# Performance work log

Measured on AMD Instinct MI355X. Metric: run time of the kernel, lower is better.

Reference implementation:

```python
import jax, jax.numpy as jnp
import numpy as np

B, S, D, H = 2, 2048, 1024, 16
DH = D // H
EPS = 1e-5


def setup_inputs() -> dict:
    key = jax.random.key(0)
    ks = jax.random.split(key, 12)
    inp = {
        "Q_source": jax.random.normal(ks[0], (B, S, D), jnp.float32),
        "K_source": jax.random.normal(ks[1], (B, S, D), jnp.float32),
        "V_source": jax.random.normal(ks[2], (B, S, D), jnp.float32),
        "padding_mask": jnp.zeros((B, 1, 1, S), dtype=bool),  # no padded keys (avoids NaN rows)
        "future_mask": jnp.triu(jnp.ones((S, S), dtype=bool), k=1)[None, None],  # causal
    }
    sc = 1.0 / np.sqrt(D)
    names = ["WQ", "WK", "WV", "WO"]
    for i, n in enumerate(names):
        inp[n] = jax.random.normal(ks[3 + i], (D, D), jnp.float32) * sc
        inp["b" + n[1]] = jnp.zeros((D,), jnp.float32)
    inp["gamma"] = jnp.ones((D,), jnp.float32)
    inp["beta"] = jnp.zeros((D,), jnp.float32)
    return inp


def reference(Q_source, K_source, V_source, padding_mask, future_mask,
              WQ, bQ, WK, bK, WV, bV, WO, bO, gamma, beta):
    b = Q_source.shape[0]
    # torch Linear: x @ W.T + b ; reshape to [B, H, S, DH]
    def proj(x, W, bb):
        y = x @ W.T + bb
        return y.reshape(b, -1, H, DH).transpose(0, 2, 1, 3)

    Q = proj(Q_source, WQ, bQ)
    K = proj(K_source, WK, bK)
    V = proj(V_source, WV, bV)

    scores = jnp.einsum("bhqd,bhkd->bhqk", Q, K) / jnp.sqrt(jnp.float32(DH))
    neg_inf = jnp.float32(-jnp.inf)
    scores = jnp.where(padding_mask, neg_inf, scores)
    scores = jnp.where(future_mask, neg_inf, scores)
    attn = jax.nn.softmax(scores, axis=-1)

    ctx = jnp.einsum("bhqk,bhkd->bhqd", attn, V)
    ctx = ctx.transpose(0, 2, 1, 3).reshape(b, -1, D)
    out = ctx @ WO.T + bO

    x = Q_source + out
    mu = x.mean(-1, keepdims=True)
    var = x.var(-1, keepdims=True)
    return (x - mu) * jax.lax.rsqrt(var + EPS) * gamma + beta
```

## Files before the change

### kernel.cpp

```cpp
#include <hip/hip_runtime.h>

#define S_LEN 2048
#define DMODEL 1024
#define NH 16
#define DHD 64

typedef __attribute__((ext_vector_type(8))) short bh8;
typedef __attribute__((ext_vector_type(4))) float f32x4;
typedef __attribute__((ext_vector_type(2))) unsigned int u32x2;
typedef __attribute__((ext_vector_type(4))) unsigned int u32x4;
typedef unsigned short u16;
typedef unsigned int u32;

static __device__ __forceinline__ u16 f2bf(float f) {
    unsigned u = __builtin_bit_cast(unsigned, f);
    u += 0x7fffu + ((u >> 16) & 1u);
    return (u16)(u >> 16);
}

typedef const __attribute__((address_space(1))) void* gptr_t;
typedef __attribute__((address_space(3))) void* lptr_t;

static __device__ __forceinline__ void gll16(const void* g, void* l) {
    __builtin_amdgcn_global_load_lds((gptr_t)g, (lptr_t)l, 16, 0, 0);
}

__global__ __launch_bounds__(256) void cvt_all(const float* __restrict__ WQ, const float* __restrict__ WK,
                                               const float* __restrict__ WV, const float* __restrict__ WO,
                                               const float* __restrict__ S0, const float* __restrict__ S1,
                                               const float* __restrict__ S2,
                                               u16* __restrict__ wq, u16* __restrict__ wk,
                                               u16* __restrict__ wv, u16* __restrict__ wo,
                                               u16* __restrict__ q0, u16* __restrict__ k0,
                                               u16* __restrict__ v0) {
    int bid = blockIdx.x;
    const float* s;
    u16* o;
    size_t base;
    if (bid < 2048) {
        int wi = bid >> 9;
        s = wi == 0 ? WQ : (wi == 1 ? WK : (wi == 2 ? WV : WO));
        o = wi == 0 ? wq : (wi == 1 ? wk : (wi == 2 ? wv : wo));
        base = (size_t)(bid & 511) * 2048;
    } else {
        int r = bid - 2048;
        int si = r >> 11;
        s = si == 0 ? S0 : (si == 1 ? S1 : S2);
        o = si == 0 ? q0 : (si == 1 ? k0 : v0);
        base = (size_t)(r & 2047) * 2048;
    }
    size_t i = base + (size_t)threadIdx.x * 8;
    float4 a = *(const float4*)(s + i);
    float4 b = *(const float4*)(s + i + 4);
    u32 p0 = (u32)f2bf(a.x) | ((u32)f2bf(a.y) << 16);
    u32 p1 = (u32)f2bf(a.z) | ((u32)f2bf(a.w) << 16);
    u32 p2 = (u32)f2bf(b.x) | ((u32)f2bf(b.y) << 16);
    u32 p3 = (u32)f2bf(b.z) | ((u32)f2bf(b.w) << 16);
    *(u32x4*)(o + i) = (u32x4){p0, p1, p2, p3};
}

template <int BM, int OBF, int AF32>
static __device__ __forceinline__ void gemm_body(const void* __restrict__ Ap, const u16* __restrict__ Bm,
                                                 const float* __restrict__ bias, void* __restrict__ Cv,
                                                 int N, int K, int bi, int bj, short* Al, short* Bl,
                                                 float oscale) {
    constexpr int MI = BM / 32;
    constexpr int NC = BM / 64;
    int tid = threadIdx.x, lane = tid & 63, w = tid >> 6;
    int ln = lane & 15, hi = lane >> 4;
    int wm = w >> 1, wn = w & 1;
    f32x4 acc[MI][4];
#pragma unroll
    for (int i = 0; i < MI; i++)
#pragma unroll
        for (int j = 0; j < 4; j++) acc[i][j] = (f32x4){0.f, 0.f, 0.f, 0.f};
    int nk = K >> 5;

    float4 fa[NC][2];
    auto loadA = [&](int kt) {
#pragma unroll
        for (int c = 0; c < NC; ++c) {
            int o = c * 4096 + tid * 16;
            int row = o >> 6, e0 = (o & 63) >> 1;
            const float* src = (const float*)Ap + (size_t)(bi * BM + row) * K + kt * 32 + e0;
            fa[c][0] = *(const float4*)src;
            fa[c][1] = *(const float4*)(src + 4);
        }
    };
    auto writeA = [&](int buf) {
#pragma unroll
        for (int c = 0; c < NC; ++c) {
            int o = c * 4096 + tid * 16;
            u32 w0 = (u32)f2bf(fa[c][0].x) | ((u32)f2bf(fa[c][0].y) << 16);
            u32 w1 = (u32)f2bf(fa[c][0].z) | ((u32)f2bf(fa[c][0].w) << 16);
            u32 w2 = (u32)f2bf(fa[c][1].x) | ((u32)f2bf(fa[c][1].y) << 16);
            u32 w3 = (u32)f2bf(fa[c][1].z) | ((u32)f2bf(fa[c][1].w) << 16);
            *(u32x4*)((char*)(Al + buf * (BM * 32)) + o) = (u32x4){w0, w1, w2, w3};
        }
    };
    auto stageA_lds = [&](int buf, int kt) {
#pragma unroll
        for (int c = 0; c < NC; ++c) {
            int o = c * 4096 + tid * 16;
            int row = o >> 6, col = (o & 63) >> 1;
            gll16((const u16*)Ap + (size_t)(bi * BM + row) * K + kt * 32 + col,
                  (char*)(Al + buf * (BM * 32)) + o);
        }
    };
    auto stageB = [&](int buf, int kt) {
#pragma unroll
        for (int c = 0; c < 2; ++c) {
            int o = c * 4096 + tid * 16;
            int row = o >> 6, col = (o & 63) >> 1;
            gll16(Bm + (size_t)(bj * 128 + row) * K + kt * 32 + col, (char*)(Bl + buf * 4096) + o);
        }
    };

    if constexpr (AF32) { loadA(0); writeA(0); } else { stageA_lds(0, 0); }
    stageB(0, 0);
    __syncthreads();
    int cur = 0;
    for (int kt = 0; kt < nk; ++kt) {
        bool pre = (kt + 1 < nk);
        if (pre) {
            if constexpr (AF32) loadA(kt + 1); else stageA_lds(cur ^ 1, kt + 1);
            stageB(cur ^ 1, kt + 1);
        }
        bh8 av[MI], bv[4];
#pragma unroll
        for (int i = 0; i < MI; i++) av[i] = *(const bh8*)&Al[cur * (BM * 32) + (wm * (BM / 2) + i * 16 + ln) * 32 + hi * 8];
#pragma unroll
        for (int j = 0; j < 4; j++) bv[j] = *(const bh8*)&Bl[cur * 4096 + (wn * 64 + j * 16 + ln) * 32 + hi * 8];
#pragma unroll
        for (int i = 0; i < MI; i++)
#pragma unroll
            for (int j = 0; j < 4; j++)
                acc[i][j] = __builtin_amdgcn_mfma_f32_16x16x32_bf16(av[i], bv[j], acc[i][j], 0, 0, 0);
        if constexpr (AF32) { if (pre) writeA(cur ^ 1); }
        __syncthreads();
        cur ^= 1;
    }
    if constexpr (OBF == 2) {
#pragma unroll
        for (int j = 0; j < 4; j++) {
            int col = wn * 64 + j * 16 + ln;
            float bvs = bias[bj * 128 + col];
#pragma unroll
            for (int i = 0; i < MI; i++) {
                int row0 = wm * (BM / 2) + i * 16 + hi * 4;
                u32 p01 = (u32)f2bf(acc[i][j][0] + bvs) | ((u32)f2bf(acc[i][j][1] + bvs) << 16);
                u32 p23 = (u32)f2bf(acc[i][j][2] + bvs) | ((u32)f2bf(acc[i][j][3] + bvs) << 16);
                int idx = col * 128 + (row0 ^ ((col & 7) << 3));
                *(u32x2*)&Al[idx] = (u32x2){p01, p23};
            }
        }
        __syncthreads();
        int b = bi >> 4;
        int sbase = (bi & 15) * 128;
#pragma unroll
        for (int it = 0; it < 8; ++it) {
            int idx = it * 256 + tid;
            int dcol = idx >> 4;
            int sl = (idx & 15) * 8;
            bh8 v = *(const bh8*)&Al[dcol * 128 + (sl ^ ((dcol & 7) << 3))];
            int h = bj * 2 + (dcol >> 6), d = dcol & 63;
            *(bh8*)((u16*)Cv + ((size_t)((b * 16 + h) * 64 + d)) * 2048 + sbase + sl) = v;
        }
        return;
    }
#pragma unroll
    for (int j = 0; j < 4; j++) {
        int col = bj * 128 + wn * 64 + j * 16 + ln;
        float bvs = bias[col];
#pragma unroll
        for (int i = 0; i < MI; i++) {
            int row0 = bi * BM + wm * (BM / 2) + i * 16 + hi * 4;
#pragma unroll
            for (int rr = 0; rr < 4; rr++) {
                if (OBF) {
                    float v = (acc[i][j][rr] + bvs) * oscale;
                    ((u16*)Cv)[(size_t)(row0 + rr) * N + col] = f2bf(v);
                } else {
                    ((float*)Cv)[(size_t)(row0 + rr) * N + col] = acc[i][j][rr] + bvs;
                }
            }
        }
    }
}

__global__ __launch_bounds__(256, 3) void gemm_qkv(const u16* __restrict__ A0, const u16* __restrict__ A1,
                                                   const u16* __restrict__ A2, const u16* __restrict__ B0,
                                                   const u16* __restrict__ B1, const u16* __restrict__ B2,
                                                   const float* __restrict__ c0, const float* __restrict__ c1,
                                                   const float* __restrict__ c2, u16* __restrict__ C0,
                                                   u16* __restrict__ C1, u16* __restrict__ VT) {
    __shared__ short SH[16384];
    short* Al = SH;
    short* Bl = SH + 8192;
    int bid = blockIdx.x;
    int swz = (bid & 7) * 96 + (bid >> 3);
    int z = swz >> 8, t = swz & 255;
    if (z == 2) {
        gemm_body<128, 2, 0>(A2, B2, c2, VT, 1024, 1024, t >> 3, t & 7, Al, Bl, 1.0f);
    } else if (z == 0) {
        gemm_body<128, 1, 0>(A0, B0, c0, C0, 1024, 1024, t >> 3, t & 7, Al, Bl, 0.18033688f);
    } else {
        gemm_body<128, 1, 0>(A1, B1, c1, C1, 1024, 1024, t >> 3, t & 7, Al, Bl, 1.0f);
    }
}

__global__ __launch_bounds__(256) void gemm_o(const u16* __restrict__ A, const u16* __restrict__ Bm,
                                              const float* __restrict__ bias, float* __restrict__ C) {
    __shared__ short Al[2 * 64 * 32];
    __shared__ short Bl[2 * 128 * 32];
    int bid = blockIdx.x;
    int swz = (bid & 7) * 64 + (bid >> 3);
    gemm_body<64, 0, 0>(A, Bm, bias, C, 1024, 1024, swz >> 3, swz & 7, Al, Bl, 1.0f);
}

template <int PLO, int PHI>
static __device__ __forceinline__ void attn_core(const u16* __restrict__ Qp, const u16* __restrict__ Kp,
                                                 const u16* __restrict__ VT, u16* __restrict__ Ctx,
                                                 short* Klb, short* Vlb, short* Pw,
                                                 int b, int h, int bh, int qt, int tid) {
    int lane = tid & 63, w = tid >> 6;
    int ln = lane & 15, hi = lane >> 4;
    __builtin_amdgcn_s_setprio(PLO);
    bh8 ones;
#pragma unroll
    for (int e = 0; e < 8; e++) ones[e] = (short)0x3F80;

    auto stage_kv = [&](int buf, int kt) {
#pragma unroll
        for (int c = 0; c < 2; ++c) {
            int o = c * 4096 + tid * 16;
            int r = o >> 7;
            int slot = (o >> 4) & 7;
            gll16(Kp + ((size_t)(b * S_LEN + kt * 64 + r)) * DMODEL + h * DHD + ((slot ^ (r & 7)) << 3),
                  (char*)(Klb + buf * 4096) + o);
            gll16(VT + ((size_t)(bh * DHD + r)) * S_LEN + kt * 64 + ((slot ^ (r & 7)) << 3),
                  (char*)(Vlb + buf * 4096) + o);
        }
    };

    int nt = qt + 1;
    int qg = (qt << 6) + w * 16 + ln;
    const bh8* qrow = (const bh8*)(Qp + ((size_t)(b * S_LEN + qg)) * DMODEL + h * DHD);
    bh8 qf0 = qrow[hi], qf1 = qrow[4 + hi];
    f32x4 ctxa[4];
    f32x4 lacc = (f32x4){0.f, 0.f, 0.f, 0.f};
#pragma unroll
    for (int i = 0; i < 4; i++) ctxa[i] = (f32x4){0.f, 0.f, 0.f, 0.f};
    stage_kv(0, 0);
    __syncthreads();
    int cur = 0;
    for (int kt = 0; kt < nt; ++kt) {
        if (kt + 1 < nt) stage_kv(cur ^ 1, kt + 1);
        f32x4 sc[4];
#pragma unroll
        for (int ks = 0; ks < 4; ++ks) sc[ks] = (f32x4){0.f, 0.f, 0.f, 0.f};
        __builtin_amdgcn_s_setprio(PHI);
#pragma unroll
        for (int dwin = 0; dwin < 2; ++dwin) {
            bh8 qv = dwin ? qf1 : qf0;
#pragma unroll
            for (int ks = 0; ks < 4; ++ks) {
                int r = ks * 16 + ln;
                bh8 kv = *(const bh8*)&Klb[cur * 4096 + r * 64 + ((dwin * 32 + hi * 8) ^ ((r & 7) << 3))];
                sc[ks] = __builtin_amdgcn_mfma_f32_16x16x32_bf16(kv, qv, sc[ks], 0, 0, 0);
            }
        }
        __builtin_amdgcn_s_setprio(PLO);
        if (kt == nt - 1) {
#pragma unroll
            for (int ks = 0; ks < 4; ++ks)
#pragma unroll
                for (int rr = 0; rr < 4; ++rr) {
                    int kg = kt * 64 + ks * 16 + hi * 4 + rr;
                    sc[ks][rr] = (kg <= qg) ? sc[ks][rr] : -1e30f;
                }
        }
#pragma unroll
        for (int ks = 0; ks < 4; ++ks) {
            u32 u0 = __builtin_bit_cast(u32, __builtin_amdgcn_exp2f(sc[ks][0]));
            u32 u1 = __builtin_bit_cast(u32, __builtin_amdgcn_exp2f(sc[ks][1]));
            u32 u2 = __builtin_bit_cast(u32, __builtin_amdgcn_exp2f(sc[ks][2]));
            u32 u3 = __builtin_bit_cast(u32, __builtin_amdgcn_exp2f(sc[ks][3]));
            u32 a01 = (u0 >> 16) | (u1 & 0xffff0000u);
            u32 a23 = (u2 >> 16) | (u3 & 0xffff0000u);
            int kloc = ks * 16 + hi * 4;
            *(u32x2*)&Pw[ln * 64 + (kloc ^ ((ln & 7) << 3))] = (u32x2){a01, a23};
        }
        __builtin_amdgcn_s_setprio(PHI);
#pragma unroll
        for (int kw = 0; kw < 2; ++kw) {
            bh8 pf = *(const bh8*)&Pw[ln * 64 + ((kw * 32 + hi * 8) ^ ((ln & 7) << 3))];
            lacc = __builtin_amdgcn_mfma_f32_16x16x32_bf16(ones, pf, lacc, 0, 0, 0);
#pragma unroll
            for (int ds = 0; ds < 4; ++ds) {
                int d = ds * 16 + ln;
                bh8 vf = *(const bh8*)&Vlb[cur * 4096 + d * 64 + ((kw * 32 + hi * 8) ^ ((d & 7) << 3))];
                ctxa[ds] = __builtin_amdgcn_mfma_f32_16x16x32_bf16(vf, pf, ctxa[ds], 0, 0, 0);
            }
        }
        __builtin_amdgcn_s_setprio(PLO);
        __syncthreads();
        cur ^= 1;
    }
    float inv = 1.f / lacc[0];
    u16* cp = Ctx + ((size_t)(b * S_LEN + qg)) * DMODEL + h * DHD;
#pragma unroll
    for (int ds = 0; ds < 4; ++ds) {
        ushort4 st;
        st.x = f2bf(ctxa[ds][0] * inv);
        st.y = f2bf(ctxa[ds][1] * inv);
        st.z = f2bf(ctxa[ds][2] * inv);
        st.w = f2bf(ctxa[ds][3] * inv);
        *(ushort4*)(cp + ds * 16 + hi * 4) = st;
    }
    __builtin_amdgcn_s_setprio(0);
}

__global__ __launch_bounds__(256) void attn_fwd(const u16* __restrict__ Qp, const u16* __restrict__ Kp,
                                                const u16* __restrict__ VT, u16* __restrict__ Ctx) {
    __shared__ short Kl[2][64 * 64];
    __shared__ short Vl[2][64 * 64];
    __shared__ short Pl[4][16 * 64];
    int tid = threadIdx.x, w = tid >> 6;
    int bid = blockIdx.x;
    int xcd = bid & 7, j = bid >> 3;
    int rnd = j >> 5, cu = j & 31;
    int bh = xcd * 4 + (cu >> 4) + ((rnd >> 1) << 1);
    int qe = cu & 15;
    int qt = (rnd & 1) ? (31 - 2 * qe) : (2 * qe);
    int b = bh >> 4, h = bh & 15;
    if (qt >= 16)
        attn_core<2, 3>(Qp, Kp, VT, Ctx, &Kl[0][0], &Vl[0][0], &Pl[w][0], b, h, bh, qt, tid);
    else
        attn_core<0, 1>(Qp, Kp, VT, Ctx, &Kl[0][0], &Vl[0][0], &Pl[w][0], b, h, bh, qt, tid);
}

__global__ __launch_bounds__(256) void ln_res(const float* __restrict__ Xres, const float* __restrict__ Y,
                                              const float* __restrict__ gamma, const float* __restrict__ beta,
                                              float* __restrict__ out) {
    int row = blockIdx.x, tid = threadIdx.x;
    const float4* xr = (const float4*)(Xres + (size_t)row * DMODEL);
    const float4* yr = (const float4*)(Y + (size_t)row * DMODEL);
    float4 a = xr[tid], bq = yr[tid];
    float x0 = a.x + bq.x, x1 = a.y + bq.y, x2 = a.z + bq.z, x3 = a.w + bq.w;
    float s1 = x0 + x1 + x2 + x3;
    float s2 = x0 * x0 + x1 * x1 + x2 * x2 + x3 * x3;
#pragma unroll
    for (int off = 32; off > 0; off >>= 1) {
        s1 += __shfl_xor(s1, off);
        s2 += __shfl_xor(s2, off);
    }
    __shared__ float r1[4], r2[4];
    int wv = tid >> 6;
    if ((tid & 63) == 0) { r1[wv] = s1; r2[wv] = s2; }
    __syncthreads();
    s1 = r1[0] + r1[1] + r1[2] + r1[3];
    s2 = r2[0] + r2[1] + r2[2] + r2[3];
    float mu = s1 * (1.0f / 1024.0f);
    float var = s2 * (1.0f / 1024.0f) - mu * mu;
    float rstd = rsqrtf(var + 1e-5f);
    const float4* g4 = (const float4*)gamma;
    const float4* b4 = (const float4*)beta;
    float4 g = g4[tid], bb = b4[tid];
    float4 res;
    res.x = (x0 - mu) * rstd * g.x + bb.x;
    res.y = (x1 - mu) * rstd * g.y + bb.y;
    res.z = (x2 - mu) * rstd * g.z + bb.z;
    res.w = (x3 - mu) * rstd * g.w + bb.w;
    *((float4*)(out + (size_t)row * DMODEL) + tid) = res;
}

extern "C" void kernel_launch(void* const* d_in, const int* in_sizes, int n_in,
                              void* d_out, int out_size, void* d_ws, size_t ws_size,
                              hipStream_t stream) {
    const float* Qs = (const float*)d_in[0];
    const float* Ks = (const float*)d_in[1];
    const float* Vs = (const float*)d_in[2];
    const float* WQ = (const float*)d_in[5];
    const float* bQ = (const float*)d_in[6];
    const float* WK = (const float*)d_in[7];
    const float* bK = (const float*)d_in[8];
    const float* WV = (const float*)d_in[9];
    const float* bV = (const float*)d_in[10];
    const float* WO = (const float*)d_in[11];
    const float* bO = (const float*)d_in[12];
    const float* gamma = (const float*)d_in[13];
    const float* beta = (const float*)d_in[14];

    const size_t MB = 1u << 20;
    char* w8 = (char*)d_ws;
    u16* Qb  = (u16*)(w8 + 0 * MB);
    u16* Kb  = (u16*)(w8 + 8 * MB);
    u16* Vb  = (u16*)(w8 + 16 * MB);
    u16* WQb = (u16*)(w8 + 24 * MB);
    u16* WKb = (u16*)(w8 + 26 * MB);
    u16* WVb = (u16*)(w8 + 28 * MB);
    u16* WOb = (u16*)(w8 + 30 * MB);
    u16* Qp  = (u16*)(w8 + 32 * MB);
    u16* Kp  = (u16*)(w8 + 40 * MB);
    u16* VTb = (u16*)(w8 + 56 * MB);
    u16* Ctx = (u16*)(w8 + 64 * MB);
    float* Y2 = (float*)(w8 + 72 * MB);

    cvt_all<<<8192, 256, 0, stream>>>(WQ, WK, WV, WO, Qs, Ks, Vs, WQb, WKb, WVb, WOb, Qb, Kb, Vb);
    gemm_qkv<<<768, 256, 0, stream>>>(Qb, Kb, Vb, WQb, WKb, WVb, bQ, bK, bV, Qp, Kp, VTb);
    attn_fwd<<<1024, 256, 0, stream>>>(Qp, Kp, VTb, Ctx);
    gemm_o<<<512, 256, 0, stream>>>(Ctx, WOb, bO, Y2);
    ln_res<<<4096, 256, 0, stream>>>(Qs, Y2, gamma, beta, (float*)d_out);
}
```

Measured before the change: 115.8 us.

## Double query rows per attention block to reuse staged K/V tiles

Each attention block now handles 128 query rows instead of 64, with every wave computing two 16-row groups. Each K/V tile staged into LDS therefore feeds twice as many MFMAs. The grid is halved to 512 blocks, the block-to-(head, q-tile) mapping is remapped, the causal mask is applied on the last two key tiles, and launch bounds request 2 blocks per CU. The cost is more registers and a larger P buffer in LDS, fewer blocks to balance the causal workload, and coarser tail imbalance.

```diff
diff --git a/kernel.cpp b/kernel.cpp
--- a/kernel.cpp
+++ b/kernel.cpp
@@ -243,98 +243,120 @@
         }
     };
 
-    int nt = qt + 1;
-    int qg = (qt << 6) + w * 16 + ln;
-    const bh8* qrow = (const bh8*)(Qp + ((size_t)(b * S_LEN + qg)) * DMODEL + h * DHD);
-    bh8 qf0 = qrow[hi], qf1 = qrow[4 + hi];
-    f32x4 ctxa[4];
-    f32x4 lacc = (f32x4){0.f, 0.f, 0.f, 0.f};
-#pragma unroll
-    for (int i = 0; i < 4; i++) ctxa[i] = (f32x4){0.f, 0.f, 0.f, 0.f};
+    int nt = 2 * qt + 2;
+    int qg0 = (qt << 7) + w * 32 + ln;
+    const bh8* qr0 = (const bh8*)(Qp + ((size_t)(b * S_LEN + qg0)) * DMODEL + h * DHD);
+    const bh8* qr1 = (const bh8*)(Qp + ((size_t)(b * S_LEN + qg0 + 16)) * DMODEL + h * DHD);
+    bh8 qf[2][2];
+    qf[0][0] = qr0[hi]; qf[0][1] = qr0[4 + hi];
+    qf[1][0] = qr1[hi]; qf[1][1] = qr1[4 + hi];
+    f32x4 ctxa[2][4];
+    f32x4 lacc[2];
+#pragma unroll
+    for (int g = 0; g < 2; g++) {
+        lacc[g] = (f32x4){0.f, 0.f, 0.f, 0.f};
+#pragma unroll
+        for (int i = 0; i < 4; i++) ctxa[g][i] = (f32x4){0.f, 0.f, 0.f, 0.f};
+    }
     stage_kv(0, 0);
     __syncthreads();
     int cur = 0;
     for (int kt = 0; kt < nt; ++kt) {
         if (kt + 1 < nt) stage_kv(cur ^ 1, kt + 1);
-        f32x4 sc[4];
-#pragma unroll
-        for (int ks = 0; ks < 4; ++ks) sc[ks] = (f32x4){0.f, 0.f, 0.f, 0.f};
+        f32x4 sc[2][4];
+#pragma unroll
+        for (int g = 0; g < 2; g++)
+#pragma unroll
+            for (int ks = 0; ks < 4; ++ks) sc[g][ks] = (f32x4){0.f, 0.f, 0.f, 0.f};
         __builtin_amdgcn_s_setprio(PHI);
 #pragma unroll
         for (int dwin = 0; dwin < 2; ++dwin) {
-            bh8 qv = dwin ? qf1 : qf0;
 #pragma unroll
             for (int ks = 0; ks < 4; ++ks) {
                 int r = ks * 16 + ln;
                 bh8 kv = *(const bh8*)&Klb[cur * 4096 + r * 64 + ((dwin * 32 + hi * 8) ^ ((r & 7) << 3))];
-                sc[ks] = __builtin_amdgcn_mfma_f32_16x16x32_bf16(kv, qv, sc[ks], 0, 0, 0);
+                sc[0][ks] = __builtin_amdgcn_mfma_f32_16x16x32_bf16(kv, qf[0][dwin], sc[0][ks], 0, 0, 0);
+                sc[1][ks] = __builtin_amdgcn_mfma_f32_16x16x32_bf16(kv, qf[1][dwin], sc[1][ks], 0, 0, 0);
             }
         }
         __builtin_amdgcn_s_setprio(PLO);
-        if (kt == nt - 1) {
-#pragma unroll
-            for (int ks = 0; ks < 4; ++ks)
-#pragma unroll
-                for (int rr = 0; rr < 4; ++rr) {
-                    int kg = kt * 64 + ks * 16 + hi * 4 + rr;
-                    sc[ks][rr] = (kg <= qg) ? sc[ks][rr] : -1e30f;
-                }
-        }
-#pragma unroll
-        for (int ks = 0; ks < 4; ++ks) {
-            u32 u0 = __builtin_bit_cast(u32, __builtin_amdgcn_exp2f(sc[ks][0]));
-            u32 u1 = __builtin_bit_cast(u32, __builtin_amdgcn_exp2f(sc[ks][1]));
-            u32 u2 = __builtin_bit_cast(u32, __builtin_amdgcn_exp2f(sc[ks][2]));
-            u32 u3 = __builtin_bit_cast(u32, __builtin_amdgcn_exp2f(sc[ks][3]));
-            u32 a01 = (u0 >> 16) | (u1 & 0xffff0000u);
-            u32 a23 = (u2 >> 16) | (u3 & 0xffff0000u);
-            int kloc = ks * 16 + hi * 4;
-            *(u32x2*)&Pw[ln * 64 + (kloc ^ ((ln & 7) << 3))] = (u32x2){a01, a23};
+        if (kt >= nt - 2) {
+#pragma unroll
+            for (int g = 0; g < 2; g++) {
+                int qgq = qg0 + g * 16;
+#pragma unroll
+                for (int ks = 0; ks < 4; ++ks)
+#pragma unroll
+                    for (int rr = 0; rr < 4; ++rr) {
+                        int kg = kt * 64 + ks * 16 + hi * 4 + rr;
+                        sc[g][ks][rr] = (kg <= qgq) ? sc[g][ks][rr] : -1e30f;
+                    }
+            }
+        }
+#pragma unroll
+        for (int g = 0; g < 2; g++) {
+#pragma unroll
+            for (int ks = 0; ks < 4; ++ks) {
+                u32 u0 = __builtin_bit_cast(u32, __builtin_amdgcn_exp2f(sc[g][ks][0]));
+                u32 u1 = __builtin_bit_cast(u32, __builtin_amdgcn_exp2f(sc[g][ks][1]));
+                u32 u2 = __builtin_bit_cast(u32, __builtin_amdgcn_exp2f(sc[g][ks][2]));
+                u32 u3 = __builtin_bit_cast(u32, __builtin_amdgcn_exp2f(sc[g][ks][3]));
+                u32 a01 = (u0 >> 16) | (u1 & 0xffff0000u);
+                u32 a23 = (u2 >> 16) | (u3 & 0xffff0000u);
+                int kloc = ks * 16 + hi * 4;
+                *(u32x2*)&Pw[(g * 16 + ln) * 64 + (kloc ^ ((ln & 7) << 3))] = (u32x2){a01, a23};
+            }
         }
         __builtin_amdgcn_s_setprio(PHI);
 #pragma unroll
         for (int kw = 0; kw < 2; ++kw) {
-            bh8 pf = *(const bh8*)&Pw[ln * 64 + ((kw * 32 + hi * 8) ^ ((ln & 7) << 3))];
-            lacc = __builtin_amdgcn_mfma_f32_16x16x32_bf16(ones, pf, lacc, 0, 0, 0);
+            bh8 pf0 = *(const bh8*)&Pw[ln * 64 + ((kw * 32 + hi * 8) ^ ((ln & 7) << 3))];
+            bh8 pf1 = *(const bh8*)&Pw[(16 + ln) * 64 + ((kw * 32 + hi * 8) ^ ((ln & 7) << 3))];
+            lacc[0] = __builtin_amdgcn_mfma_f32_16x16x32_bf16(ones, pf0, lacc[0], 0, 0, 0);
+            lacc[1] = __builtin_amdgcn_mfma_f32_16x16x32_bf16(ones, pf1, lacc[1], 0, 0, 0);
 #pragma unroll
             for (int ds = 0; ds < 4; ++ds) {
                 int d = ds * 16 + ln;
                 bh8 vf = *(const bh8*)&Vlb[cur * 4096 + d * 64 + ((kw * 32 + hi * 8) ^ ((d & 7) << 3))];
-                ctxa[ds] = __builtin_amdgcn_mfma_f32_16x16x32_bf16(vf, pf, ctxa[ds], 0, 0, 0);
+                ctxa[0][ds] = __builtin_amdgcn_mfma_f32_16x16x32_bf16(vf, pf0, ctxa[0][ds], 0, 0, 0);
+                ctxa[1][ds] = __builtin_amdgcn_mfma_f32_16x16x32_bf16(vf, pf1, ctxa[1][ds], 0, 0, 0);
             }
         }
         __builtin_amdgcn_s_setprio(PLO);
         __syncthreads();
         cur ^= 1;
     }
-    float inv = 1.f / lacc[0];
-    u16* cp = Ctx + ((size_t)(b * S_LEN + qg)) * DMODEL + h * DHD;
-#pragma unroll
-    for (int ds = 0; ds < 4; ++ds) {
-        ushort4 st;
-        st.x = f2bf(ctxa[ds][0] * inv);
-        st.y = f2bf(ctxa[ds][1] * inv);
-        st.z = f2bf(ctxa[ds][2] * inv);
-        st.w = f2bf(ctxa[ds][3] * inv);
-        *(ushort4*)(cp + ds * 16 + hi * 4) = st;
+#pragma unroll
+    for (int g = 0; g < 2; g++) {
+        float inv = 1.f / lacc[g][0];
+        u16* cp = Ctx + ((size_t)(b * S_LEN + qg0 + g * 16)) * DMODEL + h * DHD;
+#pragma unroll
+        for (int ds = 0; ds < 4; ++ds) {
+            ushort4 st;
+            st.x = f2bf(ctxa[g][ds][0] * inv);
+            st.y = f2bf(ctxa[g][ds][1] * inv);
+            st.z = f2bf(ctxa[g][ds][2] * inv);
+            st.w = f2bf(ctxa[g][ds][3] * inv);
+            *(ushort4*)(cp + ds * 16 + hi * 4) = st;
+        }
     }
     __builtin_amdgcn_s_setprio(0);
 }
 
-__global__ __launch_bounds__(256) void attn_fwd(const u16* __restrict__ Qp, const u16* __restrict__ Kp,
-                                                const u16* __restrict__ VT, u16* __restrict__ Ctx) {
+__global__ __launch_bounds__(256, 2) void attn_fwd(const u16* __restrict__ Qp, const u16* __restrict__ Kp,
+                                                   const u16* __restrict__ VT, u16* __restrict__ Ctx) {
     __shared__ short Kl[2][64 * 64];
     __shared__ short Vl[2][64 * 64];
-    __shared__ short Pl[4][16 * 64];
+    __shared__ short Pl[4][32 * 64];
     int tid = threadIdx.x, w = tid >> 6;
     int bid = blockIdx.x;
     int xcd = bid & 7, j = bid >> 3;
     int rnd = j >> 5, cu = j & 31;
-    int bh = xcd * 4 + (cu >> 4) + ((rnd >> 1) << 1);
-    int qe = cu & 15;
-    int qt = (rnd & 1) ? (31 - 2 * qe) : (2 * qe);
+    int bh = xcd * 4 + rnd * 2 + (cu >> 4);
+    int qtl = cu & 15;
+    int qt = rnd ? (15 - qtl) : qtl;
     int b = bh >> 4, h = bh & 15;
-    if (qt >= 16)
+    if (qt >= 8)
         attn_core<2, 3>(Qp, Kp, VT, Ctx, &Kl[0][0], &Vl[0][0], &Pl[w][0], b, h, bh, qt, tid);
     else
         attn_core<0, 1>(Qp, Kp, VT, Ctx, &Kl[0][0], &Vl[0][0], &Pl[w][0], b, h, bh, qt, tid);
@@ -409,7 +431,7 @@
 
     cvt_all<<<8192, 256, 0, stream>>>(WQ, WK, WV, WO, Qs, Ks, Vs, WQb, WKb, WVb, WOb, Qb, Kb, Vb);
     gemm_qkv<<<768, 256, 0, stream>>>(Qb, Kb, Vb, WQb, WKb, WVb, bQ, bK, bV, Qp, Kp, VTb);
-    attn_fwd<<<1024, 256, 0, stream>>>(Qp, Kp, VTb, Ctx);
+    attn_fwd<<<512, 256, 0, stream>>>(Qp, Kp, VTb, Ctx);
     gemm_o<<<512, 256, 0, stream>>>(Ctx, WOb, bO, Y2);
     ln_res<<<4096, 256, 0, stream>>>(Qs, Y2, gamma, beta, (float*)d_out);
 }
```

Result: slower. 119.2 us (+2.9%).
